# Performance work log

Measured on AMD Instinct MI355X. Metric: run time of the kernel, lower is better.

Reference implementation:

```python
import jax, jax.numpy as jnp
import numpy as np

DIM = 1024
N_HEADS = 16
N_KV_HEADS = 4
HEAD_DIM = DIM // N_HEADS
N_REP = N_HEADS // N_KV_HEADS
N_EXPERTS = 4
TOP_K = 2
HIDDEN = 3 * DIM
EPS = 1.1920928955078125e-07  # torch RMSNorm default eps = finfo(float32).eps


def setup_inputs() -> dict:
    key = jax.random.key(0)
    ks = jax.random.split(key, 12)
    s = 0.02
    B, S = 2, 2048
    return {
        "x": jax.random.normal(ks[0], (B, S, DIM), jnp.float32),
        "g1": jnp.ones((DIM,), jnp.float32),
        "g2": jnp.ones((DIM,), jnp.float32),
        "wq": jax.random.normal(ks[1], (DIM, N_HEADS * HEAD_DIM), jnp.float32) * s,
        "wk": jax.random.normal(ks[2], (DIM, N_KV_HEADS * HEAD_DIM), jnp.float32) * s,
        "wv": jax.random.normal(ks[3], (DIM, N_KV_HEADS * HEAD_DIM), jnp.float32) * s,
        "wo": jax.random.normal(ks[4], (N_HEADS * HEAD_DIM, DIM), jnp.float32) * s,
        "gate": jax.random.normal(ks[5], (DIM, N_EXPERTS), jnp.float32) * s,
        "w1": jax.random.normal(ks[6], (N_EXPERTS, DIM, HIDDEN), jnp.float32) * s,
        "w2": jax.random.normal(ks[7], (N_EXPERTS, HIDDEN, DIM), jnp.float32) * s,
        "w3": jax.random.normal(ks[8], (N_EXPERTS, DIM, HIDDEN), jnp.float32) * s,
    }


def _rmsnorm(x, g):
    var = jnp.mean(jnp.square(x), axis=-1, keepdims=True)
    return x * jax.lax.rsqrt(var + EPS) * g


def _rotate_half(x):
    x1, x2 = jnp.split(x, 2, axis=-1)
    return jnp.concatenate([-x2, x1], axis=-1)


def _rope_tables(S):
    inv_freq = 1.0 / (10000.0 ** (jnp.arange(0, HEAD_DIM, 2, dtype=jnp.float32) / HEAD_DIM))
    freqs = jnp.arange(S, dtype=jnp.float32)[:, None] * inv_freq[None, :]  # [S, hd/2]
    emb = jnp.concatenate([freqs, freqs], axis=-1)  # [S, hd]
    return jnp.cos(emb), jnp.sin(emb)


def _attention(x, wq, wk, wv, wo):
    B, S, D = x.shape
    q = (x @ wq).reshape(B, S, N_HEADS, HEAD_DIM).transpose(0, 2, 1, 3)      # [B,H,S,hd]
    k = (x @ wk).reshape(B, S, N_KV_HEADS, HEAD_DIM).transpose(0, 2, 1, 3)   # [B,Hkv,S,hd]
    v = (x @ wv).reshape(B, S, N_KV_HEADS, HEAD_DIM).transpose(0, 2, 1, 3)
    cos, sin = _rope_tables(S)
    q = q * cos + _rotate_half(q) * sin
    k = k * cos + _rotate_half(k) * sin
    k = jnp.repeat(k, N_REP, axis=1)  # [B,H,S,hd]
    v = jnp.repeat(v, N_REP, axis=1)
    scores = jnp.einsum("bhqd,bhkd->bhqk", q, k) / jnp.sqrt(jnp.float32(HEAD_DIM))
    causal = jnp.tril(jnp.ones((S, S), dtype=bool))
    scores = jnp.where(causal, scores, -jnp.inf)
    attn = jax.nn.softmax(scores, axis=-1)
    out = jnp.einsum("bhqk,bhkd->bhqd", attn, v)
    return out.transpose(0, 2, 1, 3).reshape(B, S, D) @ wo


def _moe(x, gate, w1, w2, w3):
    B, S, D = x.shape
    xf = x.reshape(-1, D)  # [N,D]
    probs = jax.nn.softmax(xf @ gate, axis=-1)
    w, idx = jax.lax.top_k(probs, TOP_K)            # [N,k]
    w = w / jnp.sum(w, axis=-1, keepdims=True)
    oh = jax.nn.one_hot(idx, N_EXPERTS, dtype=xf.dtype)  # [N,k,E]
    comb = jnp.einsum("nk,nke->ne", w, oh)               # [N,E] per-expert weight
    out = jnp.zeros_like(xf)
    for e in range(N_EXPERTS):
        h = jax.nn.silu(xf @ w1[e]) * (xf @ w3[e])
        out = out + comb[:, e:e + 1] * (h @ w2[e])
    return out.reshape(B, S, D)


def reference(x, g1, g2, wq, wk, wv, wo, gate, w1, w2, w3):
    x = x + _attention(_rmsnorm(x, g1), wq, wk, wv, wo)
    x = x + _moe(_rmsnorm(x, g2), gate, w1, w2, w3)
    return x
```

## Files before the change

kernel.cpp:

```cpp
#include <hip/hip_runtime.h>
#include <stdint.h>

#define DIMD 1024
#define NH 16
#define NKV 4
#define HD 64
#define NEXP 4
#define HID 3072
#define BB 2
#define SS 2048
#define NT (BB*SS)
#define EPSF 1.1920928955078125e-07f
#define LOG2E 1.4426950408889634f

typedef short short8 __attribute__((ext_vector_type(8)));
typedef short short4v __attribute__((ext_vector_type(4)));
typedef float f32x4 __attribute__((ext_vector_type(4)));

__device__ __forceinline__ short f2bf(float f) {
  union { float f; unsigned u; } c; c.f = f;
  unsigned u = c.u;
  unsigned r = u + 0x7fffu + ((u >> 16) & 1u);
  return (short)(r >> 16);
}
__device__ __forceinline__ float bf2f(short s) {
  union { unsigned u; float f; } c;
  c.u = ((unsigned)(unsigned short)s) << 16;
  return c.f;
}
__device__ __forceinline__ float fexp2(float x) {
#if __has_builtin(__builtin_amdgcn_exp2f)
  return __builtin_amdgcn_exp2f(x);
#else
  return exp2f(x);
#endif
}

__device__ __forceinline__ f32x4 mfma16(short8 a, short8 b, f32x4 c) {
  return __builtin_amdgcn_mfma_f32_16x16x32_bf16(a, b, c, 0, 0, 0);
}

#define GLOAD16(gp, lp) __builtin_amdgcn_global_load_lds( \
    (const __attribute__((address_space(1))) void*)(gp),  \
    (__attribute__((address_space(3))) void*)(lp), 16, 0, 0)

template<int SPLIT>
__global__ __launch_bounds__(256) void transpose_k(
    const float* __restrict__ in, short* __restrict__ o1, short* __restrict__ o2,
    int Krows, int N, size_t inStride, size_t outStride, int ldo1, int ldo2,
    int mapMode) {
  __shared__ float tile[64][68];
  const float* inp = in + (size_t)blockIdx.z * inStride;
  short* hp = o1 + (size_t)blockIdx.z * outStride;
  short* lp = SPLIT ? (o2 + (size_t)blockIdx.z * outStride) : (short*)0;
  int tx = threadIdx.x & 15, ty = threadIdx.x >> 4;
  int n0 = blockIdx.x * 64, k0 = blockIdx.y * 64;
#pragma unroll
  for (int p = 0; p < 4; ++p) {
    int k = p * 16 + ty;
    float4 v = *(const float4*)&inp[(size_t)(k0 + k) * N + n0 + tx * 4];
    *(float4*)&tile[k][tx * 4] = v;
  }
  __syncthreads();
#pragma unroll
  for (int p = 0; p < 4; ++p) {
    int n = n0 + p * 16 + ty;
    int np = mapMode ? ((n >> 4) * 32 + (n & 15) + ((mapMode == 2) ? 16 : 0)) : n;
    int k4 = tx * 4;
    short4v hv, lv;
#pragma unroll
    for (int j = 0; j < 4; ++j) {
      float v = tile[k4 + j][p * 16 + ty];
      short h_ = f2bf(v);
      hv[j] = h_;
      if (SPLIT) lv[j] = f2bf(v - bf2f(h_));
    }
    *(short4v*)&hp[(size_t)np * ldo1 + k0 + k4] = hv;
    if (SPLIT) *(short4v*)&lp[(size_t)np * ldo2 + k0 + k4] = lv;
  }
}

__global__ __launch_bounds__(256) void rmsnorm_k(
    const float* __restrict__ x, const float* __restrict__ g, short* __restrict__ outq) {
  int row = blockIdx.x;
  int t = threadIdx.x;
  const float4* xr = (const float4*)(x + (size_t)row * DIMD);
  float4 v = xr[t];
  float ss = v.x*v.x + v.y*v.y + v.z*v.z + v.w*v.w;
#pragma unroll
  for (int off = 1; off < 64; off <<= 1) ss += __shfl_xor(ss, off);
  __shared__ float red[4];
  if ((t & 63) == 0) red[t >> 6] = ss;
  __syncthreads();
  float tot = red[0] + red[1] + red[2] + red[3];
  float scn = rsqrtf(tot * (1.f/1024.f) + EPSF);
  float4 gv = ((const float4*)g)[t];
  short4v ov;
  ov[0] = f2bf(v.x * scn * gv.x);
  ov[1] = f2bf(v.y * scn * gv.y);
  ov[2] = f2bf(v.z * scn * gv.z);
  ov[3] = f2bf(v.w * scn * gv.w);
  ((short4v*)outq)[(size_t)row * 256 + t] = ov;
}

__global__ __launch_bounds__(256) void rope_tables_k(
    float* __restrict__ cosT, float* __restrict__ sinT) {
  int t = blockIdx.x * 256 + threadIdx.x;
  int s = t >> 5, i = t & 31;
  float invf = powf(10000.0f, -(float)i / 32.0f);
  float a = (float)s * invf;
  cosT[t] = cosf(a);
  sinT[t] = sinf(a);
}

#define QSCALE 0.18033688011112042f
__global__ __launch_bounds__(256) void rope_scatter_k(
    const float* __restrict__ qkv, const float* __restrict__ cosT,
    const float* __restrict__ sinT, short* __restrict__ Qb,
    short* __restrict__ Kb, short* __restrict__ Vt) {
  int r = blockIdx.x;
  int t = threadIdx.x;
  int b = r >> 11, s = r & 2047;
  __shared__ float row[1536];
  const float* rp = qkv + (size_t)r * 1536;
  for (int i = t; i < 1536; i += 256) row[i] = rp[i];
  __syncthreads();
  const float* cs = cosT + s * 32;
  const float* sn = sinT + s * 32;
  {
    int c = t * 4, hh = c >> 6, j = c & 63;
    short4v ov;
#pragma unroll
    for (int u = 0; u < 4; ++u) {
      int jj = j + u;
      float xv = row[hh*64 + jj];
      float rot = (jj < 32) ? -row[hh*64 + jj + 32] : row[hh*64 + jj - 32];
      ov[u] = f2bf((xv * cs[jj & 31] + rot * sn[jj & 31]) * QSCALE);
    }
    *(short4v*)&Qb[((size_t)(b*NH + hh) * SS + s) * 64 + j] = ov;
  }
  if (t < 64) {
    int c = t * 4, kvh = c >> 6, j = c & 63;
    short4v ov;
#pragma unroll
    for (int u = 0; u < 4; ++u) {
      int jj = j + u;
      float xv = row[1024 + kvh*64 + jj];
      float rot = (jj < 32) ? -row[1024 + kvh*64 + jj + 32] : row[1024 + kvh*64 + jj - 32];
      ov[u] = f2bf(xv * cs[jj & 31] + rot * sn[jj & 31]);
    }
    *(short4v*)&Kb[((size_t)(b*NKV + kvh) * SS + s) * 64 + j] = ov;
  } else if (t < 128) {
    int c = (t - 64) * 4, kvh = c >> 6, j = c & 63;
#pragma unroll
    for (int u = 0; u < 4; ++u)
      Vt[((size_t)(b*NKV + kvh) * 64 + j + u) * SS + s] = f2bf(row[1280 + kvh*64 + j + u]);
  }
}

template<int EPI, int AFOLD>
__global__ __launch_bounds__(256, 2) void gemm_bt(
    const short* __restrict__ A, const short* __restrict__ Bt,
    float* __restrict__ C, short* __restrict__ Cb,
    const float* __restrict__ R,
    const int* __restrict__ idx, const int* __restrict__ meta,
    const float* __restrict__ comb,
    int M, int N, int K, int lda, int ldb) {
  __shared__ short As[128*64];
  __shared__ short Bs[128*64];
  int nx = gridDim.x, ny = gridDim.y;
  int nwg = nx * ny * gridDim.z;
  int o = blockIdx.x + nx * (blockIdx.y + ny * blockIdx.z);
  int xcd = o & 7, loc = o >> 3;
  int q = nwg >> 3, rr = nwg & 7;
  int wg = (xcd < rr ? xcd * (q + 1) : rr * (q + 1) + (xcd - rr) * q) + loc;
  int bm = wg % nx; int t1 = wg / nx; int bn = t1 % ny; int bz = t1 / ny;
  int tid = threadIdx.x;
  int w = tid >> 6, lane = tid & 63;
  int m0 = bm * 128, n0 = bn * 128;
  int cnt = M, abase = 0, eidx = 0, hrow0 = 0;
  const int* list = idx;
  if (EPI == 7) {
    const int* mp = meta + bz * 4;
    cnt = mp[1]; hrow0 = mp[2];
    list = idx + bz * 4096;
    Bt += (size_t)bz * 6144 * ldb;
    if (m0 >= cnt) return;
  }
  if (EPI == 6) {
    eidx = bz >> 1; int slot = bz & 1;
    const int* mp = meta + eidx * 4;
    int cA = mp[0], cT = mp[1];
    cnt = slot ? (cT - cA) : cA;
    abase = mp[2] + (slot ? cA : 0);
    list = idx + eidx * 4096 + (slot ? cA : 0);
    Bt += (size_t)eidx * 1024 * ldb;
    if (m0 >= cnt) return;
  }
  int wr = (w >> 1) * 64, wc = (w & 1) * 64;
  int l15 = lane & 15, lg = lane >> 4;
  int srow = lane >> 3, sslot = lane & 7;
  const short* aptr[4];
  const short* bptr[4];
#pragma unroll
  for (int i = 0; i < 4; ++i) {
    int row = i * 32 + w * 8 + srow;
    int gs = (sslot ^ (row & 7)) * 8;
    int am = m0 + row;
    if (EPI == 7) am = list[am < cnt ? am : cnt - 1];
    else if (EPI == 6) am = abase + am;
    aptr[i] = A + (size_t)am * lda + gs;
    bptr[i] = Bt + (size_t)(n0 + row) * ldb + gs;
  }
  f32x4 acc[4][4] = {};
  int nK = K >> 6;
  for (int kt = 0; kt < nK; ++kt) {
    int k0 = kt << 6;
    int ak0 = AFOLD ? (kt < 16 ? k0 : k0 - 1024) : k0;
    __syncthreads();
#pragma unroll
    for (int i = 0; i < 4; ++i) {
      int r0 = i * 32 + w * 8;
      GLOAD16(aptr[i] + ak0, &As[r0 * 64]);
      GLOAD16(bptr[i] + k0, &Bs[r0 * 64]);
    }
    asm volatile("s_waitcnt vmcnt(0)" ::: "memory");
    __syncthreads();
#pragma unroll
    for (int kh = 0; kh < 2; ++kh) {
      short8 af[4], bfv[4];
#pragma unroll
      for (int mi = 0; mi < 4; ++mi) {
        int row = wr + mi * 16 + l15;
        int sl = (lg + kh * 4) ^ (row & 7);
        af[mi] = *(const short8*)&As[row * 64 + sl * 8];
        int rowb = wc + mi * 16 + l15;
        int slb = (lg + kh * 4) ^ (rowb & 7);
        bfv[mi] = *(const short8*)&Bs[rowb * 64 + slb * 8];
      }
#pragma unroll
      for (int mi = 0; mi < 4; ++mi)
#pragma unroll
        for (int ni = 0; ni < 4; ++ni)
          acc[mi][ni] = mfma16(af[mi], bfv[ni], acc[mi][ni]);
    }
  }
#pragma unroll
  for (int mi = 0; mi < 4; ++mi) {
#pragma unroll
    for (int i = 0; i < 4; ++i) {
      int m = m0 + wr + mi * 16 + 4 * lg + i;
      if (EPI == 7) {
        if (m < cnt) {
          int g0 = (n0 + wc) >> 5;
#pragma unroll
          for (int p = 0; p < 2; ++p) {
            float xg = acc[mi][2*p][i];
            float yg = acc[mi][2*p+1][i];
            float sg = 1.f / (1.f + fexp2(-xg * LOG2E));
            Cb[(size_t)(hrow0 + m) * 3072 + (g0 + p) * 16 + l15] = f2bf(xg * sg * yg);
          }
        }
      } else if (EPI == 6) {
        if (m < cnt) {
          int tok = list[m];
          float wgt = comb[tok * 4 + eidx];
#pragma unroll
          for (int ni = 0; ni < 4; ++ni) {
            int n = n0 + wc + ni * 16 + l15;
            atomicAdd(&C[(size_t)tok * 1024 + n], wgt * acc[mi][ni][i]);
          }
        }
      } else {
#pragma unroll
        for (int ni = 0; ni < 4; ++ni) {
          int n = n0 + wc + ni * 16 + l15;
          size_t cidx = (size_t)m * N + n;
          float v = acc[mi][ni][i];
          if (EPI == 0)      C[cidx] = v;
          else               C[cidx] = v + R[cidx];
        }
      }
    }
  }
}

__global__ __launch_bounds__(512) void attn_k(
    const short* __restrict__ Qb, const short* __restrict__ Kb,
    const short* __restrict__ Vt, short* __restrict__ AO2) {
  int id = blockIdx.x;
  int qp = ((id & 15) + ((id >> 8) << 3)) & 15;
  int hb = (id >> 4) & 31;
  int h = hb & 15, b = hb >> 4;
  int tid = threadIdx.x;
  int w = tid >> 6, lane = tid & 63;
  int half = w >> 2, w4 = w & 3;
  int l15 = lane & 15, lg = lane >> 4;
  int kvh = h >> 2;
  __shared__ short Ks[64 * 64];
  __shared__ short Vs[64 * 64];
  __shared__ short P[8][16 * 72];
  short* Pw = P[w];
  const short* Qp = Qb + (size_t)(b * NH + h) * SS * 64;
  const short* Kp = Kb + (size_t)(b * NKV + kvh) * SS * 64;
  const short* Vp = Vt + (size_t)(b * NKV + kvh) * 64 * SS;
  int qt = half ? (31 - qp) : qp;
  int kmax = 31 - qp;
  int qbase = qt * 64 + w4 * 16;
  int qrow0 = qbase + 4 * lg;
  short8 aq0 = *(const short8*)&Qp[(size_t)(qbase + l15) * 64 + 8 * lg];
  short8 aq1 = *(const short8*)&Qp[(size_t)(qbase + l15) * 64 + 8 * lg + 32];
  int srow = lane >> 3, sslot = lane & 7;
  int strow = w * 8 + srow;
  int sgs = (sslot ^ (strow & 7)) * 8;
  const short* ksrc = Kp + (size_t)strow * 64 + sgs;
  const short* vsrc = Vp + (size_t)strow * SS + sgs;
  f32x4 o4[4] = {};
  float lst[4] = {0.f, 0.f, 0.f, 0.f};
  for (int kt = 0; kt <= kmax; ++kt) {
    int k0 = kt * 64;
    __syncthreads();
    GLOAD16(ksrc + (size_t)k0 * 64, &Ks[(w * 8) * 64]);
    GLOAD16(vsrc + k0, &Vs[(w * 8) * 64]);
    asm volatile("s_waitcnt vmcnt(0)" ::: "memory");
    __syncthreads();
    if (kt <= qt) {
      f32x4 sc[4] = {};
      short8 bk[2][4];
#pragma unroll
      for (int kh = 0; kh < 2; ++kh)
#pragma unroll
        for (int ni = 0; ni < 4; ++ni) {
          int row = ni * 16 + l15;
          int sl = (lg + kh * 4) ^ (row & 7);
          bk[kh][ni] = *(const short8*)&Ks[row * 64 + sl * 8];
        }
      __builtin_amdgcn_s_setprio(1);
#pragma unroll
      for (int kh = 0; kh < 2; ++kh)
#pragma unroll
        for (int ni = 0; ni < 4; ++ni)
          sc[ni] = mfma16(kh ? aq1 : aq0, bk[kh][ni], sc[ni]);
      __builtin_amdgcn_s_setprio(0);
      short8 bv[2][4];
#pragma unroll
      for (int kh = 0; kh < 2; ++kh)
#pragma unroll
        for (int di = 0; di < 4; ++di) {
          int row = di * 16 + l15;
          int sl = (lg + kh * 4) ^ (row & 7);
          bv[kh][di] = *(const short8*)&Vs[row * 64 + sl * 8];
        }
      if (kt == qt) {
#pragma unroll
        for (int ni = 0; ni < 4; ++ni)
#pragma unroll
          for (int i = 0; i < 4; ++i)
            if (k0 + ni*16 + l15 > qrow0 + i) sc[ni][i] = -3.0e38f;
      }
#pragma unroll
      for (int i = 0; i < 4; ++i) {
        float ps = 0.f;
#pragma unroll
        for (int ni = 0; ni < 4; ++ni) {
          float pv = fexp2(sc[ni][i]);
          sc[ni][i] = pv;
          ps += pv;
        }
        lst[i] += ps;
      }
#pragma unroll
      for (int ni = 0; ni < 4; ++ni)
#pragma unroll
        for (int i = 0; i < 4; ++i)
          Pw[(4*lg + i) * 72 + ni*16 + l15] = f2bf(sc[ni][i]);
      __builtin_amdgcn_s_setprio(1);
#pragma unroll
      for (int kh = 0; kh < 2; ++kh) {
        short8 ap = *(const short8*)&Pw[l15 * 72 + 8*lg + 32*kh];
#pragma unroll
        for (int di = 0; di < 4; ++di)
          o4[di] = mfma16(ap, bv[kh][di], o4[di]);
      }
      __builtin_amdgcn_s_setprio(0);
    }
  }
  float rinv[4];
#pragma unroll
  for (int i = 0; i < 4; ++i) {
    float s = lst[i];
    s += __shfl_xor(s, 1); s += __shfl_xor(s, 2);
    s += __shfl_xor(s, 4); s += __shfl_xor(s, 8);
    rinv[i] = 1.f / s;
  }
#pragma unroll
  for (int di = 0; di < 4; ++di) {
#pragma unroll
    for (int i = 0; i < 4; ++i) {
      float val = o4[di][i] * rinv[i];
      short hi_ = f2bf(val);
      short lo_ = f2bf(val - bf2f(hi_));
      size_t idx = ((size_t)(b * SS + qrow0 + i)) * 2048 + h*64 + di*16 + l15;
      AO2[idx] = hi_;
      AO2[idx + 1024] = lo_;
    }
  }
}

__global__ __launch_bounds__(64) void routing_k(
    const float* __restrict__ x1, const float* __restrict__ g2,
    const float* __restrict__ gate, float* __restrict__ comb, int* __restrict__ rsel) {
  int row = blockIdx.x;
  int l = threadIdx.x;
  const float* xr = x1 + (size_t)row * 1024;
  float ss = 0.f;
  float lgt[4] = {0.f, 0.f, 0.f, 0.f};
  for (int it = 0; it < 4; ++it) {
    int d0 = it * 256 + l * 4;
    float4 v = *(const float4*)&xr[d0];
    float4 gv = *(const float4*)&g2[d0];
    const float* vp = (const float*)&v;
    const float* gp = (const float*)&gv;
#pragma unroll
    for (int u = 0; u < 4; ++u) {
      float xv = vp[u];
      ss += xv * xv;
      float xg = xv * gp[u];
      float4 gr = *(const float4*)&gate[(size_t)(d0 + u) * 4];
      lgt[0] += xg * gr.x; lgt[1] += xg * gr.y;
      lgt[2] += xg * gr.z; lgt[3] += xg * gr.w;
    }
  }
#pragma unroll
  for (int off = 1; off < 64; off <<= 1) {
    ss += __shfl_xor(ss, off);
#pragma unroll
    for (int e = 0; e < 4; ++e) lgt[e] += __shfl_xor(lgt[e], off);
  }
  if (l == 0) {
    float scn = rsqrtf(ss * (1.f/1024.f) + EPSF);
    float lmax = fmaxf(fmaxf(lgt[0], lgt[1]), fmaxf(lgt[2], lgt[3]));
    float p[4];
#pragma unroll
    for (int e = 0; e < 4; ++e) p[e] = expf(scn * (lgt[e] - lmax));
    int i1 = 0;
    for (int e = 1; e < 4; ++e) if (p[e] > p[i1]) i1 = e;
    int i2 = (i1 == 0) ? 1 : 0;
    for (int e = 0; e < 4; ++e) if (e != i1 && p[e] > p[i2]) i2 = e;
    float wsum = p[i1] + p[i2];
    float4 ov = {0.f, 0.f, 0.f, 0.f};
    ((float*)&ov)[i1] = p[i1] / wsum;
    ((float*)&ov)[i2] = p[i2] / wsum;
    *(float4*)&comb[(size_t)row * 4] = ov;
    rsel[row] = i1 * 4 + i2;
  }
}

__global__ __launch_bounds__(1024) void compact_k(
    const int* __restrict__ rsel, int* __restrict__ idxb, int* __restrict__ meta) {
  int e = blockIdx.x;
  int t = threadIdx.x;
  int lane = t & 63, wid = t >> 6;
  int base = t * 4;
  int r[4];
#pragma unroll
  for (int j = 0; j < 4; ++j) r[j] = rsel[base + j];
  __shared__ int wsum[16], woff[16], totA;
  int outb = e * 4096;
#pragma unroll
  for (int pass = 0; pass < 2; ++pass) {
    int loc[4], c = 0;
#pragma unroll
    for (int j = 0; j < 4; ++j) {
      int sel = pass ? (r[j] & 3) : (r[j] >> 2);
      loc[j] = (sel == e) ? 1 : 0;
      c += loc[j];
    }
    int v = c;
#pragma unroll
    for (int off = 1; off < 64; off <<= 1) {
      int o = __shfl_up(v, off);
      if (lane >= off) v += o;
    }
    if (lane == 63) wsum[wid] = v;
    __syncthreads();
    if (t < 16) {
      int s = wsum[t];
      int vv = s;
#pragma unroll
      for (int off = 1; off < 16; off <<= 1) {
        int o = __shfl_up(vv, off);
        if (t >= off) vv += o;
      }
      woff[t] = vv - s;
      if (t == 15) {
        if (pass == 0) { totA = vv; meta[e * 4 + 0] = vv; }
        else           { meta[e * 4 + 1] = totA + vv; }
      }
    }
    __syncthreads();
    int pbase = (pass ? totA : 0) + woff[wid] + (v - c);
#pragma unroll
    for (int j = 0; j < 4; ++j)
      if (loc[j]) idxb[outb + pbase++] = base + j;
    __syncthreads();
  }
}

__global__ void eoff_k(int* __restrict__ meta) {
  if (threadIdx.x == 0 && blockIdx.x == 0) {
    int run = 0;
    for (int e = 0; e < 4; ++e) { meta[e * 4 + 2] = run; run += meta[e * 4 + 1]; }
  }
}

extern "C" void kernel_launch(void* const* d_in, const int* in_sizes, int n_in,
                              void* d_out, int out_size, void* d_ws, size_t ws_size,
                              hipStream_t stream) {
  const float* x    = (const float*)d_in[0];
  const float* g1   = (const float*)d_in[1];
  const float* g2   = (const float*)d_in[2];
  const float* wq   = (const float*)d_in[3];
  const float* wk   = (const float*)d_in[4];
  const float* wv   = (const float*)d_in[5];
  const float* wo   = (const float*)d_in[6];
  const float* gate = (const float*)d_in[7];
  const float* w1   = (const float*)d_in[8];
  const float* w2   = (const float*)d_in[9];
  const float* w3   = (const float*)d_in[10];
  float* out = (float*)d_out;

  char* p = (char*)d_ws;
  size_t off = 0;
  auto carve = [&](size_t bytes) {
    void* r = p + off;
    off = (off + bytes + 255) & ~(size_t)255;
    return r;
  };
  short* wqkvT = (short*)carve((size_t)1536 * 1024 * 2);
  short* woC3  = (short*)carve((size_t)1024 * 3072 * 2);
  short* w13T  = (short*)carve((size_t)NEXP * 6144 * 1024 * 2);
  short* w2T   = (short*)carve((size_t)NEXP * 1024 * 3072 * 2);
  short* xn1   = (short*)carve((size_t)NT * DIMD * 2);
  short* xn2   = (short*)carve((size_t)NT * DIMD * 2);
  float* qkv   = (float*)carve((size_t)NT * 1536 * 4);
  float* cosT  = (float*)carve((size_t)SS * 32 * 4);
  float* sinT  = (float*)carve((size_t)SS * 32 * 4);
  short* Qb    = (short*)carve((size_t)BB * NH * SS * HD * 2);
  short* Kb    = (short*)carve((size_t)BB * NKV * SS * HD * 2);
  short* Vt    = (short*)carve((size_t)BB * NKV * HD * SS * 2);
  short* AO2   = (short*)carve((size_t)NT * 2048 * 2);
  float* comb  = (float*)carve((size_t)NT * 4 * 4);
  int*   rsel  = (int*)carve((size_t)NT * 4);
  int*   idxb  = (int*)carve((size_t)NEXP * 4096 * 4);
  int*   meta  = (int*)carve((size_t)16 * 4);
  short* Hb    = (short*)carve((size_t)(2 * NT + 256) * 3072 * 2);
  (void)ws_size; (void)in_sizes; (void)n_in; (void)out_size;

  dim3 blk(256);
  transpose_k<0><<<dim3(16, 16), blk, 0, stream>>>(wq, wqkvT, (short*)0, 1024, 1024, 0, 0, 1024, 0, 0);
  transpose_k<0><<<dim3(4, 16), blk, 0, stream>>>(wk, wqkvT + (size_t)1024 * 1024, (short*)0, 1024, 256, 0, 0, 1024, 0, 0);
  transpose_k<0><<<dim3(4, 16), blk, 0, stream>>>(wv, wqkvT + (size_t)1280 * 1024, (short*)0, 1024, 256, 0, 0, 1024, 0, 0);
  transpose_k<1><<<dim3(16, 16), blk, 0, stream>>>(wo, woC3, woC3 + 1024, 1024, 1024, 0, 0, 3072, 3072, 0);
  transpose_k<0><<<dim3(16, 16), blk, 0, stream>>>(wo, woC3 + 2048, (short*)0, 1024, 1024, 0, 0, 3072, 0, 0);
  transpose_k<0><<<dim3(48, 16, 4), blk, 0, stream>>>(w1, w13T, (short*)0, 1024, 3072, (size_t)1024*3072, (size_t)6144*1024, 1024, 0, 1);
  transpose_k<0><<<dim3(48, 16, 4), blk, 0, stream>>>(w3, w13T, (short*)0, 1024, 3072, (size_t)1024*3072, (size_t)6144*1024, 1024, 0, 2);
  transpose_k<0><<<dim3(16, 48, 4), blk, 0, stream>>>(w2, w2T, (short*)0, 3072, 1024, (size_t)3072*1024, (size_t)1024*3072, 3072, 0, 0);
  rope_tables_k<<<dim3(256), blk, 0, stream>>>(cosT, sinT);

  rmsnorm_k<<<dim3(NT), blk, 0, stream>>>(x, g1, xn1);
  gemm_bt<0,0><<<dim3(32, 12), blk, 0, stream>>>(xn1, wqkvT, qkv, (short*)0, (const float*)0,
      (const int*)0, (const int*)0, (const float*)0, NT, 1536, 1024, 1024, 1024);
  rope_scatter_k<<<dim3(NT), blk, 0, stream>>>(qkv, cosT, sinT, Qb, Kb, Vt);
  attn_k<<<dim3(512), dim3(512), 0, stream>>>(Qb, Kb, Vt, AO2);
  gemm_bt<1,1><<<dim3(32, 8), blk, 0, stream>>>(AO2, woC3, out, (short*)0, x,
      (const int*)0, (const int*)0, (const float*)0, NT, 1024, 3072, 2048, 3072);

  rmsnorm_k<<<dim3(NT), blk, 0, stream>>>(out, g2, xn2);
  routing_k<<<dim3(NT), dim3(64), 0, stream>>>(out, g2, gate, comb, rsel);
  compact_k<<<dim3(4), dim3(1024), 0, stream>>>(rsel, idxb, meta);
  eoff_k<<<dim3(1), dim3(64), 0, stream>>>(meta);
  gemm_bt<7,0><<<dim3(32, 48, 4), blk, 0, stream>>>(xn2, w13T, (float*)0, Hb, (const float*)0,
      idxb, meta, (const float*)0, NT, 6144, 1024, 1024, 1024);
  gemm_bt<6,0><<<dim3(32, 8, 8), blk, 0, stream>>>(Hb, w2T, out, (short*)0, (const float*)0,
      idxb, meta, comb, NT, 1024, 3072, 3072, 3072);
}
```

Measured before the change: 478.0 us.

## Double-buffer attention K/V tiles and fuse second RMSNorm and expert offsets

The attention kernel now double-buffers its K/V shared-memory tiles. It prefetches the next tile while computing on the current one, with one barrier per iteration instead of two, so global load latency can be hidden. Separately, the second RMSNorm is folded into the routing kernel, which now writes the bf16 normalized activations. The compaction kernel runs all experts in a single block and computes the expert offsets, which removes the rmsnorm and eoff launches. The costs are double the LDS use for K/V in attention, which may lower occupancy, and serialized compaction across experts in one block.

```diff
diff --git a/kernel.cpp b/kernel.cpp
--- a/kernel.cpp
+++ b/kernel.cpp
@@ -297,8 +297,8 @@
   int half = w >> 2, w4 = w & 3;
   int l15 = lane & 15, lg = lane >> 4;
   int kvh = h >> 2;
-  __shared__ short Ks[64 * 64];
-  __shared__ short Vs[64 * 64];
+  __shared__ short Ks[2][64 * 64];
+  __shared__ short Vs[2][64 * 64];
   __shared__ short P[8][16 * 72];
   short* Pw = P[w];
   const short* Qp = Qb + (size_t)(b * NH + h) * SS * 64;
@@ -317,14 +317,21 @@
   const short* vsrc = Vp + (size_t)strow * SS + sgs;
   f32x4 o4[4] = {};
   float lst[4] = {0.f, 0.f, 0.f, 0.f};
+  GLOAD16(ksrc, &Ks[0][(w * 8) * 64]);
+  GLOAD16(vsrc, &Vs[0][(w * 8) * 64]);
+  asm volatile("s_waitcnt vmcnt(0)" ::: "memory");
+  __builtin_amdgcn_s_barrier();
   for (int kt = 0; kt <= kmax; ++kt) {
-    int k0 = kt * 64;
-    __syncthreads();
-    GLOAD16(ksrc + (size_t)k0 * 64, &Ks[(w * 8) * 64]);
-    GLOAD16(vsrc + k0, &Vs[(w * 8) * 64]);
-    asm volatile("s_waitcnt vmcnt(0)" ::: "memory");
-    __syncthreads();
+    int cur = kt & 1;
+    if (kt < kmax) {
+      int k1 = (kt + 1) * 64;
+      GLOAD16(ksrc + (size_t)k1 * 64, &Ks[cur ^ 1][(w * 8) * 64]);
+      GLOAD16(vsrc + k1, &Vs[cur ^ 1][(w * 8) * 64]);
+    }
     if (kt <= qt) {
+      int k0 = kt * 64;
+      const short* Kc = &Ks[cur][0];
+      const short* Vc = &Vs[cur][0];
       f32x4 sc[4] = {};
       short8 bk[2][4];
 #pragma unroll
@@ -333,7 +340,7 @@
         for (int ni = 0; ni < 4; ++ni) {
           int row = ni * 16 + l15;
           int sl = (lg + kh * 4) ^ (row & 7);
-          bk[kh][ni] = *(const short8*)&Ks[row * 64 + sl * 8];
+          bk[kh][ni] = *(const short8*)&Kc[row * 64 + sl * 8];
         }
       __builtin_amdgcn_s_setprio(1);
 #pragma unroll
@@ -349,7 +356,7 @@
         for (int di = 0; di < 4; ++di) {
           int row = di * 16 + l15;
           int sl = (lg + kh * 4) ^ (row & 7);
-          bv[kh][di] = *(const short8*)&Vs[row * 64 + sl * 8];
+          bv[kh][di] = *(const short8*)&Vc[row * 64 + sl * 8];
         }
       if (kt == qt) {
 #pragma unroll
@@ -384,6 +391,8 @@
       }
       __builtin_amdgcn_s_setprio(0);
     }
+    asm volatile("s_waitcnt vmcnt(0) lgkmcnt(0)" ::: "memory");
+    __builtin_amdgcn_s_barrier();
   }
   float rinv[4];
 #pragma unroll
@@ -409,7 +418,8 @@
 
 __global__ __launch_bounds__(64) void routing_k(
     const float* __restrict__ x1, const float* __restrict__ g2,
-    const float* __restrict__ gate, float* __restrict__ comb, int* __restrict__ rsel) {
+    const float* __restrict__ gate, float* __restrict__ comb,
+    int* __restrict__ rsel, short* __restrict__ xn2) {
   int row = blockIdx.x;
   int l = threadIdx.x;
   const float* xr = x1 + (size_t)row * 1024;
@@ -437,8 +447,19 @@
 #pragma unroll
     for (int e = 0; e < 4; ++e) lgt[e] += __shfl_xor(lgt[e], off);
   }
+  float scn = rsqrtf(ss * (1.f/1024.f) + EPSF);
+  for (int it = 0; it < 4; ++it) {
+    int d0 = it * 256 + l * 4;
+    float4 v = *(const float4*)&xr[d0];
+    float4 gv = *(const float4*)&g2[d0];
+    short4v ov;
+    ov[0] = f2bf(v.x * scn * gv.x);
+    ov[1] = f2bf(v.y * scn * gv.y);
+    ov[2] = f2bf(v.z * scn * gv.z);
+    ov[3] = f2bf(v.w * scn * gv.w);
+    *(short4v*)&xn2[(size_t)row * 1024 + d0] = ov;
+  }
   if (l == 0) {
-    float scn = rsqrtf(ss * (1.f/1024.f) + EPSF);
     float lmax = fmaxf(fmaxf(lgt[0], lgt[1]), fmaxf(lgt[2], lgt[3]));
     float p[4];
 #pragma unroll
@@ -458,59 +479,54 @@
 
 __global__ __launch_bounds__(1024) void compact_k(
     const int* __restrict__ rsel, int* __restrict__ idxb, int* __restrict__ meta) {
-  int e = blockIdx.x;
   int t = threadIdx.x;
   int lane = t & 63, wid = t >> 6;
   int base = t * 4;
   int r[4];
 #pragma unroll
   for (int j = 0; j < 4; ++j) r[j] = rsel[base + j];
-  __shared__ int wsum[16], woff[16], totA;
-  int outb = e * 4096;
-#pragma unroll
-  for (int pass = 0; pass < 2; ++pass) {
-    int loc[4], c = 0;
-#pragma unroll
-    for (int j = 0; j < 4; ++j) {
-      int sel = pass ? (r[j] & 3) : (r[j] >> 2);
-      loc[j] = (sel == e) ? 1 : 0;
-      c += loc[j];
-    }
-    int v = c;
-#pragma unroll
-    for (int off = 1; off < 64; off <<= 1) {
-      int o = __shfl_up(v, off);
-      if (lane >= off) v += o;
-    }
-    if (lane == 63) wsum[wid] = v;
+  __shared__ int wsum[16], woff[16], shA, shT;
+  int run = 0;
+  for (int e = 0; e < 4; ++e) {
+    int outb = e * 4096;
+#pragma unroll
+    for (int pass = 0; pass < 2; ++pass) {
+      int loc[4], c = 0;
+#pragma unroll
+      for (int j = 0; j < 4; ++j) {
+        int sel = pass ? (r[j] & 3) : (r[j] >> 2);
+        loc[j] = (sel == e) ? 1 : 0;
+        c += loc[j];
+      }
+      int v = c;
+#pragma unroll
+      for (int off = 1; off < 64; off <<= 1) {
+        int o = __shfl_up(v, off);
+        if (lane >= off) v += o;
+      }
+      if (lane == 63) wsum[wid] = v;
+      __syncthreads();
+      if (t < 16) {
+        int s = wsum[t];
+        int vv = s;
+#pragma unroll
+        for (int off = 1; off < 16; off <<= 1) {
+          int o = __shfl_up(vv, off);
+          if (t >= off) vv += o;
+        }
+        woff[t] = vv - s;
+        if (t == 15) { if (pass == 0) shA = vv; else shT = shA + vv; }
+      }
+      __syncthreads();
+      int pbase = (pass ? shA : 0) + woff[wid] + (v - c);
+#pragma unroll
+      for (int j = 0; j < 4; ++j)
+        if (loc[j]) idxb[outb + pbase++] = base + j;
+      __syncthreads();
+    }
+    if (t == 0) { meta[e*4+0] = shA; meta[e*4+1] = shT; meta[e*4+2] = run; }
+    run += shT;
     __syncthreads();
-    if (t < 16) {
-      int s = wsum[t];
-      int vv = s;
-#pragma unroll
-      for (int off = 1; off < 16; off <<= 1) {
-        int o = __shfl_up(vv, off);
-        if (t >= off) vv += o;
-      }
-      woff[t] = vv - s;
-      if (t == 15) {
-        if (pass == 0) { totA = vv; meta[e * 4 + 0] = vv; }
-        else           { meta[e * 4 + 1] = totA + vv; }
-      }
-    }
-    __syncthreads();
-    int pbase = (pass ? totA : 0) + woff[wid] + (v - c);
-#pragma unroll
-    for (int j = 0; j < 4; ++j)
-      if (loc[j]) idxb[outb + pbase++] = base + j;
-    __syncthreads();
-  }
-}
-
-__global__ void eoff_k(int* __restrict__ meta) {
-  if (threadIdx.x == 0 && blockIdx.x == 0) {
-    int run = 0;
-    for (int e = 0; e < 4; ++e) { meta[e * 4 + 2] = run; run += meta[e * 4 + 1]; }
   }
 }
 
@@ -576,10 +592,8 @@
   gemm_bt<1,1><<<dim3(32, 8), blk, 0, stream>>>(AO2, woC3, out, (short*)0, x,
       (const int*)0, (const int*)0, (const float*)0, NT, 1024, 3072, 2048, 3072);
 
-  rmsnorm_k<<<dim3(NT), blk, 0, stream>>>(out, g2, xn2);
-  routing_k<<<dim3(NT), dim3(64), 0, stream>>>(out, g2, gate, comb, rsel);
-  compact_k<<<dim3(4), dim3(1024), 0, stream>>>(rsel, idxb, meta);
-  eoff_k<<<dim3(1), dim3(64), 0, stream>>>(meta);
+  routing_k<<<dim3(NT), dim3(64), 0, stream>>>(out, g2, gate, comb, rsel, xn2);
+  compact_k<<<dim3(1), dim3(1024), 0, stream>>>(rsel, idxb, meta);
   gemm_bt<7,0><<<dim3(32, 48, 4), blk, 0, stream>>>(xn2, w13T, (float*)0, Hb, (const float*)0,
       idxb, meta, (const float*)0, NT, 6144, 1024, 1024, 1024);
   gemm_bt<6,0><<<dim3(32, 8, 8), blk, 0, stream>>>(Hb, w2T, out, (short*)0, (const float*)0,
```

Result: no change. 476.4 us (-0.3%).
